# Kernel optimization log

Hardware: AMD Instinct MI355X
Metric: run time of the kernel (lower is better)

## Reference

```python
import jax, jax.numpy as jnp
import numpy as np

NUM_GRIDS = 8

def _rbf(x):
    # FastKAN-style radial basis over a fixed grid on [-2, 2]
    grid = jnp.linspace(-2.0, 2.0, NUM_GRIDS).astype(x.dtype)
    h = 4.0 / (NUM_GRIDS - 1)  # grid spacing used as RBF bandwidth
    z = (x[..., None] - grid) / h
    return jnp.exp(-z * z)  # (..., D, G)

def _spline_layer(x, base_w, base_b, spline_w, spline_b):
    # base path: Linear(silu(x)); spline path: Linear(rbf features)
    base = jax.nn.silu(x) @ base_w.T + base_b
    feats = _rbf(x).reshape(x.shape[:-1] + (x.shape[-1] * NUM_GRIDS,))
    return base + feats @ spline_w.T + spline_b


def setup_inputs() -> dict:
    key = jax.random.key(0)
    ks = jax.random.split(key, 12)
    B, Sx, Sy, D = 4, 1024, 1024, 256
    H1, H2 = 128, 64
    def lin(k, o, i):
        return (jax.random.normal(k, (o, i), jnp.float32) / np.sqrt(i)).astype(jnp.float32)
    return {
        "x": jax.random.normal(ks[0], (B, Sx, D), jnp.float32),
        "y": jax.random.normal(ks[1], (B, Sy, D), jnp.float32),
        "base_w1x": lin(ks[2], H1, D), "base_b1x": jnp.zeros((H1,), jnp.float32),
        "spline_w1x": lin(ks[3], H1, D * NUM_GRIDS), "spline_b1x": jnp.zeros((H1,), jnp.float32),
        "base_w2x": lin(ks[4], H2, H1), "base_b2x": jnp.zeros((H2,), jnp.float32),
        "spline_w2x": lin(ks[5], H2, H1 * NUM_GRIDS), "spline_b2x": jnp.zeros((H2,), jnp.float32),
        "base_w1y": lin(ks[6], H1, D), "base_b1y": jnp.zeros((H1,), jnp.float32),
        "spline_w1y": lin(ks[7], H1, D * NUM_GRIDS), "spline_b1y": jnp.zeros((H1,), jnp.float32),
        "base_w2y": lin(ks[8], H2, H1), "base_b2y": jnp.zeros((H2,), jnp.float32),
        "spline_w2y": lin(ks[9], H2, H1 * NUM_GRIDS), "spline_b2y": jnp.zeros((H2,), jnp.float32),
        "final_w": lin(ks[10], 1, 2 * H2), "final_b": jnp.zeros((1,), jnp.float32),
    }


def reference(x, y,
              base_w1x, base_b1x, spline_w1x, spline_b1x,
              base_w2x, base_b2x, spline_w2x, spline_b2x,
              base_w1y, base_b1y, spline_w1y, spline_b1y,
              base_w2y, base_b2y, spline_w2y, spline_b2y,
              final_w, final_b):
    # Per-branch spline stacks: (B, S, D) -> (B, S, H2)
    hx = _spline_layer(_spline_layer(x, base_w1x, base_b1x, spline_w1x, spline_b1x),
                       base_w2x, base_b2x, spline_w2x, spline_b2x)
    hy = _spline_layer(_spline_layer(y, base_w1y, base_b1y, spline_w1y, spline_b1y),
                       base_w2y, base_b2y, spline_w2y, spline_b2y)
    # The original expands to (B, Sx, Sy, 2*H2), applies the affine final
    # layer, then means over all Sx*Sy pairs. By linearity this equals two
    # independent seq-means projected by the split weight, avoiding the
    # quadratic intermediate while computing identical math.
    H2 = hx.shape[-1]
    wx, wy = final_w[:, :H2], final_w[:, H2:]
    out = hx.mean(axis=1) @ wx.T + hy.mean(axis=1) @ wy.T + final_b  # (B, 1)
    return out
```

## Files before the change

kernel.cpp:

```cpp
#include <hip/hip_runtime.h>

typedef __attribute__((ext_vector_type(8))) short short8;
typedef __attribute__((ext_vector_type(8))) float floatx8;
typedef __attribute__((ext_vector_type(8))) __bf16 bf16x8;
typedef __attribute__((ext_vector_type(16))) float floatx16;


__device__ __forceinline__ unsigned short f2bf(float f) {
  union { float f; unsigned u; } v; v.f = f;
  unsigned r = v.u + 0x7fffu + ((v.u >> 16) & 1u);
  return (unsigned short)(r >> 16);
}

#define STP 33

__global__ __launch_bounds__(256) void prep_frags(
    const float* __restrict__ bw1x, const float* __restrict__ sw1x,
    const float* __restrict__ bb1x, const float* __restrict__ sb1x,
    const float* __restrict__ bw2x, const float* __restrict__ sw2x,
    const float* __restrict__ bb2x, const float* __restrict__ sb2x,
    const float* __restrict__ bw1y, const float* __restrict__ sw1y,
    const float* __restrict__ bb1y, const float* __restrict__ sb1y,
    const float* __restrict__ bw2y, const float* __restrict__ sw2y,
    const float* __restrict__ bb2y, const float* __restrict__ sb2y,
    uint4* __restrict__ B1fx, uint4* __restrict__ B1fy,
    uint4* __restrict__ B2fx, uint4* __restrict__ B2fy,
    float* __restrict__ b1x, float* __restrict__ b1y,
    float* __restrict__ b2x, float* __restrict__ b2y,
    int* __restrict__ cnt)
{
  __shared__ unsigned short stage[9 * 16 * STP];

  const int cid = blockIdx.x;
  const int t   = threadIdx.x;

  if (cid < 160) {
    const bool isB1 = (cid < 128);
    int sid, ds, nc, ostr, sstr, ncs;
    const float *bw, *sw;
    uint4* dst;
    if (isB1) {
      sid = cid >> 6; int c = cid & 63; ds = c >> 2; nc = c & 3;
      bw = sid ? bw1y : bw1x; sw = sid ? sw1y : sw1x;
      dst = sid ? B1fy : B1fx;
      ostr = 256; sstr = 2048; ncs = 4;
    } else {
      int c2 = cid - 128; sid = c2 >> 4; int c = c2 & 15; ds = c >> 1; nc = c & 1;
      bw = sid ? bw2y : bw2x; sw = sid ? sw2y : sw2x;
      dst = sid ? B2fy : B2fx;
      ostr = 128; sstr = 1024; ncs = 2;
    }
    const int o_l = t >> 3;
    const int o   = nc * 32 + o_l;
    #pragma unroll
    for (int e = 0; e < 2; ++e) {
      int dd = (t & 7) * 2 + e;
      int d  = ds * 16 + dd;
      float bwv = bw[o * ostr + d];
      stage[(0 * 16 + dd) * STP + o_l] = f2bf(bwv);
      const float* sp = sw + (size_t)o * sstr + d * 8;
      float4 s0 = *(const float4*)sp;
      float4 s1 = *(const float4*)(sp + 4);
      stage[(1 * 16 + dd) * STP + o_l] = f2bf(s0.x);
      stage[(2 * 16 + dd) * STP + o_l] = f2bf(s0.y);
      stage[(3 * 16 + dd) * STP + o_l] = f2bf(s0.z);
      stage[(4 * 16 + dd) * STP + o_l] = f2bf(s0.w);
      stage[(5 * 16 + dd) * STP + o_l] = f2bf(s1.x);
      stage[(6 * 16 + dd) * STP + o_l] = f2bf(s1.y);
      stage[(7 * 16 + dd) * STP + o_l] = f2bf(s1.z);
      stage[(8 * 16 + dd) * STP + o_l] = f2bf(s1.w);
    }
    __syncthreads();
    for (int u = t; u < 9 * 64; u += 256) {
      int j = u >> 6, l = u & 63;
      int dd0 = (l >> 5) * 8;
      int oL  = l & 31;
      unsigned short e8[8];
      #pragma unroll
      for (int i = 0; i < 8; ++i)
        e8[i] = stage[(j * 16 + dd0 + i) * STP + oL];
      uint4 oh;
      oh.x = (unsigned)e8[0] | ((unsigned)e8[1] << 16);
      oh.y = (unsigned)e8[2] | ((unsigned)e8[3] << 16);
      oh.z = (unsigned)e8[4] | ((unsigned)e8[5] << 16);
      oh.w = (unsigned)e8[6] | ((unsigned)e8[7] << 16);
      int q = (ds * 9 + j) * ncs + nc;
      dst[q * 64 + l] = oh;
    }
  } else {
    for (int i2 = t; i2 < 388; i2 += 256) {
      if (i2 < 128)      b1x[i2]       = bb1x[i2]       + sb1x[i2];
      else if (i2 < 256) b1y[i2 - 128] = bb1y[i2 - 128] + sb1y[i2 - 128];
      else if (i2 < 320) b2x[i2 - 256] = bb2x[i2 - 256] + sb2x[i2 - 256];
      else if (i2 < 384) b2y[i2 - 320] = bb2y[i2 - 320] + sb2y[i2 - 320];
      else               cnt[i2 - 384] = 0;
    }
  }
}

__global__ __launch_bounds__(512, 2) void fused_kernel(
    const float* __restrict__ Xx, const float* __restrict__ Xy,
    const uint4* __restrict__ B1fx, const uint4* __restrict__ B1fy,
    const uint4* __restrict__ B2fx, const uint4* __restrict__ B2fy,
    const float* __restrict__ b1x_, const float* __restrict__ b1y_,
    const float* __restrict__ b2x_, const float* __restrict__ b2y_,
    const float* __restrict__ finw, const float* __restrict__ finb,
    float* __restrict__ partial, int* __restrict__ cnt,
    float* __restrict__ out)
{
  __shared__ __align__(16) char smem[51232];
  float* xsh  = (float*)smem;
  float* S0   = (float*)smem;
  float* S1   = (float*)(smem + 16384);
  float* h1s  = (float*)(smem + 33792);
  float* redw = (float*)(smem + 51200);

  const int t    = threadIdx.x;
  const int bid  = blockIdx.x;
  const int sid  = bid >> 7;
  const int m    = bid & 127;
  const int wave = t >> 6;
  const int l    = t & 63;
  const int lc   = l & 31;
  const int lk   = l >> 5;

  const float* X  = sid ? Xy : Xx;
  const uint4* B1 = sid ? B1fy : B1fx;
  const uint4* B2 = sid ? B2fy : B2fx;
  const float* b1 = sid ? b1y_ : b1x_;
  const float* b2 = sid ? b2y_ : b2x_;

  {
    int row = t >> 4, col = (t & 15) * 16;
    const float* src = X + (size_t)(m * 32 + row) * 256 + col;
    #pragma unroll
    for (int q = 0; q < 4; ++q)
      *(float4*)(xsh + row * 264 + col + q * 4) = *(const float4*)(src + q * 4);
  }
  __syncthreads();

  float xr0[8], xr1[8];
  {
    int cb = wave * 32 + lk * 8;
    float4 v0 = *(const float4*)(xsh + lc * 264 + cb);
    float4 v1 = *(const float4*)(xsh + lc * 264 + cb + 4);
    float4 u0 = *(const float4*)(xsh + lc * 264 + cb + 16);
    float4 u1 = *(const float4*)(xsh + lc * 264 + cb + 20);
    xr0[0]=v0.x; xr0[1]=v0.y; xr0[2]=v0.z; xr0[3]=v0.w;
    xr0[4]=v1.x; xr0[5]=v1.y; xr0[6]=v1.z; xr0[7]=v1.w;
    xr1[0]=u0.x; xr1[1]=u0.y; xr1[2]=u0.z; xr1[3]=u0.w;
    xr1[4]=u1.x; xr1[5]=u1.y; xr1[6]=u1.z; xr1[7]=u1.w;
  }
  __syncthreads();

  floatx16 acc[4] = {};

  auto loadB1 = [&](int s, uint4* bf) {
    int j = s >> 1, ds = wave * 2 + (s & 1);
    const uint4* bp = B1 + (size_t)((ds * 9 + j) * 4) * 64 + l;
    #pragma unroll
    for (int nc = 0; nc < 4; ++nc) bf[nc] = bp[nc * 64];
  };
  auto computeB1 = [&](int s, const uint4* bf) {
    int j = s >> 1;
    const float* xr = (s & 1) ? xr1 : xr0;
    floatx8 f;
    if (j == 0) {
      #pragma unroll
      for (int i = 0; i < 8; ++i)
        f[i] = __fdividef(xr[i], 1.f + __expf(-xr[i]));
    } else {
      float g = -2.f + (float)(j - 1) * (4.f / 7.f);
      #pragma unroll
      for (int i = 0; i < 8; ++i) {
        float z = (xr[i] - g) * 1.75f;
        f[i] = __expf(-z * z);
      }
    }
    short8 a = __builtin_bit_cast(short8, __builtin_convertvector(f, bf16x8));
    #pragma unroll
    for (int nc = 0; nc < 4; ++nc) {
      short8 bh = __builtin_bit_cast(short8, bf[nc]);
      acc[nc] = __builtin_amdgcn_mfma_f32_32x32x16_bf16(a, bh, acc[nc], 0, 0, 0);
    }
  };

  {
    uint4 bfE[4], bfO[4];
    loadB1(0, bfE);
    #pragma unroll 1
    for (int s = 0; s < 18; s += 2) {
      loadB1(s + 1, bfO);
      computeB1(s, bfE);
      if (s + 2 < 18) loadB1(s + 2, bfE);
      computeB1(s + 1, bfO);
    }
  }

  auto st = [&](float* Sb) {
    #pragma unroll
    for (int nc = 0; nc < 4; ++nc)
      #pragma unroll
      for (int r = 0; r < 16; ++r) {
        int row = (r & 3) + 8 * (r >> 2) + 4 * lk;
        Sb[row * 128 + nc * 32 + lc] = acc[nc][r];
      }
  };
  auto ad = [&](const float* Sb) {
    #pragma unroll
    for (int nc = 0; nc < 4; ++nc)
      #pragma unroll
      for (int r = 0; r < 16; ++r) {
        int row = (r & 3) + 8 * (r >> 2) + 4 * lk;
        acc[nc][r] += Sb[row * 128 + nc * 32 + lc];
      }
  };
  __syncthreads();
  if (wave == 1) st(S0);
  if (wave == 3) st(S1);
  __syncthreads();
  if (wave == 0) ad(S0);
  if (wave == 2) ad(S1);
  __syncthreads();
  if (wave == 5) st(S0);
  if (wave == 7) st(S1);
  __syncthreads();
  if (wave == 4) ad(S0);
  if (wave == 6) ad(S1);
  __syncthreads();
  if (wave == 2) st(S0);
  if (wave == 6) st(S1);
  __syncthreads();
  if (wave == 0) ad(S0);
  if (wave == 4) ad(S1);
  __syncthreads();
  if (wave == 4) st(S0);
  __syncthreads();
  if (wave == 0) {
    ad(S0);
    #pragma unroll
    for (int nc = 0; nc < 4; ++nc)
      #pragma unroll
      for (int r = 0; r < 16; ++r) {
        int row = (r & 3) + 8 * (r >> 2) + 4 * lk;
        int col = nc * 32 + lc;
        h1s[row * 136 + col] = acc[nc][r] + b1[col];
      }
  }
  __syncthreads();

  floatx16 acc2[2] = {};

  auto loadB2 = [&](int s, uint4* cf) {
    const uint4* bp = B2 + (size_t)((wave * 9 + s) * 2) * 64 + l;
    #pragma unroll
    for (int nc = 0; nc < 2; ++nc) cf[nc] = bp[nc * 64];
  };

  uint4 cfE[2], cfO[2];
  loadB2(0, cfE);

  float hr[8];
  {
    int cb = wave * 16 + lk * 8;
    float4 v0 = *(const float4*)(h1s + lc * 136 + cb);
    float4 v1 = *(const float4*)(h1s + lc * 136 + cb + 4);
    hr[0]=v0.x; hr[1]=v0.y; hr[2]=v0.z; hr[3]=v0.w;
    hr[4]=v1.x; hr[5]=v1.y; hr[6]=v1.z; hr[7]=v1.w;
  }

  auto computeB2 = [&](int s, const uint4* cf) {
    floatx8 f;
    if (s == 0) {
      #pragma unroll
      for (int i = 0; i < 8; ++i)
        f[i] = __fdividef(hr[i], 1.f + __expf(-hr[i]));
    } else {
      float g = -2.f + (float)(s - 1) * (4.f / 7.f);
      #pragma unroll
      for (int i = 0; i < 8; ++i) {
        float z = (hr[i] - g) * 1.75f;
        f[i] = __expf(-z * z);
      }
    }
    short8 a = __builtin_bit_cast(short8, __builtin_convertvector(f, bf16x8));
    #pragma unroll
    for (int nc = 0; nc < 2; ++nc) {
      short8 bh = __builtin_bit_cast(short8, cf[nc]);
      acc2[nc] = __builtin_amdgcn_mfma_f32_32x32x16_bf16(a, bh, acc2[nc], 0, 0, 0);
    }
  };

  #pragma unroll 1
  for (int s = 0; s < 8; s += 2) {
    loadB2(s + 1, cfO);
    computeB2(s, cfE);
    loadB2(s + 2, cfE);
    computeB2(s + 1, cfO);
  }
  computeB2(8, cfE);

  const float* wf = finw + sid * 64;
  {
    float w0 = wf[lc], w1v = wf[32 + lc];
    float pz = 0.f;
    #pragma unroll
    for (int r = 0; r < 16; ++r) pz += acc2[0][r] * w0 + acc2[1][r] * w1v;
    #pragma unroll
    for (int off = 32; off > 0; off >>= 1) pz += __shfl_down(pz, off, 64);
    if (l == 0) redw[wave] = pz;
  }
  __syncthreads();

  if (wave == 0) {
    const int b    = m >> 5;
    const int slot = sid * 32 + (m & 31);
    float v = (l < 8) ? redw[l] : 0.f;
    v += 32.f * b2[l] * wf[l];
    #pragma unroll
    for (int off = 32; off > 0; off >>= 1) v += __shfl_down(v, off, 64);
    int old = 0;
    if (l == 0) {
      partial[b * 64 + slot] = v;
      __threadfence();
      old = atomicAdd(&cnt[b], 1);
    }
    int bc = __shfl(old, 0, 64);
    if (bc == 63) {
      float pv = atomicAdd(&partial[b * 64 + l], 0.f);
      #pragma unroll
      for (int off = 32; off > 0; off >>= 1) pv += __shfl_down(pv, off, 64);
      if (l == 0) out[b] = finb[0] + pv * (1.0f / 1024.0f);
    }
  }
}

extern "C" void kernel_launch(void* const* d_in, const int* in_sizes, int n_in,
                              void* d_out, int out_size, void* d_ws, size_t ws_size,
                              hipStream_t stream)
{
  (void)in_sizes; (void)n_in; (void)out_size; (void)ws_size;
  const float* x    = (const float*)d_in[0];
  const float* y    = (const float*)d_in[1];
  const float* bw1x = (const float*)d_in[2];
  const float* bb1x = (const float*)d_in[3];
  const float* sw1x = (const float*)d_in[4];
  const float* sb1x = (const float*)d_in[5];
  const float* bw2x = (const float*)d_in[6];
  const float* bb2x = (const float*)d_in[7];
  const float* sw2x = (const float*)d_in[8];
  const float* sb2x = (const float*)d_in[9];
  const float* bw1y = (const float*)d_in[10];
  const float* bb1y = (const float*)d_in[11];
  const float* sw1y = (const float*)d_in[12];
  const float* sb1y = (const float*)d_in[13];
  const float* bw2y = (const float*)d_in[14];
  const float* bb2y = (const float*)d_in[15];
  const float* sw2y = (const float*)d_in[16];
  const float* sb2y = (const float*)d_in[17];
  const float* finw = (const float*)d_in[18];
  const float* finb = (const float*)d_in[19];

  char* ws = (char*)d_ws;
  uint4* B1fx = (uint4*)(ws);
  uint4* B1fy = (uint4*)(ws + 589824);
  uint4* B2fx = (uint4*)(ws + 1179648);
  uint4* B2fy = (uint4*)(ws + 1327104);
  float* b1x  = (float*)(ws + 1474560);
  float* b1y  = b1x + 128;
  float* b2x  = b1y + 128;
  float* b2y  = b2x + 64;
  float* partial = b2y + 64;
  int*   cnt  = (int*)(partial + 256);

  hipLaunchKernelGGL(prep_frags, dim3(161), dim3(256), 0, stream,
                     bw1x, sw1x, bb1x, sb1x, bw2x, sw2x, bb2x, sb2x,
                     bw1y, sw1y, bb1y, sb1y, bw2y, sw2y, bb2y, sb2y,
                     B1fx, B1fy, B2fx, B2fy, b1x, b1y, b2x, b2y, cnt);

  hipLaunchKernelGGL(fused_kernel, dim3(256), dim3(512), 0, stream,
                     x, y, B1fx, B1fy, B2fx, B2fy, b1x, b1y, b2x, b2y,
                     finw, finb, partial, cnt, (float*)d_out);
}
```

Before: 30.79 us.

## Drop B-fragment double-buffering and raise occupancy to three blocks per CU

Replaces the software-pipelined, double-buffered weight fragment loads in both MFMA loops with simple per-iteration load-then-compute loops. It also raises the launch-bounds minimum blocks per CU from 2 to 3. The aim is to cut register pressure so more waves are resident and can hide load latency through occupancy rather than manual prefetch. The risk is exposed global-load latency in each iteration if occupancy does not actually rise, or spills under the tighter register budget.

```diff
diff --git a/kernel.cpp b/kernel.cpp
--- a/kernel.cpp
+++ b/kernel.cpp
@@ -98,7 +98,7 @@
   }
 }
 
-__global__ __launch_bounds__(512, 2) void fused_kernel(
+__global__ __launch_bounds__(512, 3) void fused_kernel(
     const float* __restrict__ Xx, const float* __restrict__ Xy,
     const uint4* __restrict__ B1fx, const uint4* __restrict__ B1fy,
     const uint4* __restrict__ B2fx, const uint4* __restrict__ B2fy,
@@ -155,14 +155,14 @@
 
   floatx16 acc[4] = {};
 
-  auto loadB1 = [&](int s, uint4* bf) {
+  #pragma unroll 1
+  for (int s = 0; s < 18; ++s) {
     int j = s >> 1, ds = wave * 2 + (s & 1);
     const uint4* bp = B1 + (size_t)((ds * 9 + j) * 4) * 64 + l;
+    uint4 bf[4];
     #pragma unroll
     for (int nc = 0; nc < 4; ++nc) bf[nc] = bp[nc * 64];
-  };
-  auto computeB1 = [&](int s, const uint4* bf) {
-    int j = s >> 1;
+
     const float* xr = (s & 1) ? xr1 : xr0;
     floatx8 f;
     if (j == 0) {
@@ -183,18 +183,6 @@
       short8 bh = __builtin_bit_cast(short8, bf[nc]);
       acc[nc] = __builtin_amdgcn_mfma_f32_32x32x16_bf16(a, bh, acc[nc], 0, 0, 0);
     }
-  };
-
-  {
-    uint4 bfE[4], bfO[4];
-    loadB1(0, bfE);
-    #pragma unroll 1
-    for (int s = 0; s < 18; s += 2) {
-      loadB1(s + 1, bfO);
-      computeB1(s, bfE);
-      if (s + 2 < 18) loadB1(s + 2, bfE);
-      computeB1(s + 1, bfO);
-    }
   }
 
   auto st = [&](float* Sb) {
@@ -250,15 +238,6 @@
   __syncthreads();
 
   floatx16 acc2[2] = {};
-
-  auto loadB2 = [&](int s, uint4* cf) {
-    const uint4* bp = B2 + (size_t)((wave * 9 + s) * 2) * 64 + l;
-    #pragma unroll
-    for (int nc = 0; nc < 2; ++nc) cf[nc] = bp[nc * 64];
-  };
-
-  uint4 cfE[2], cfO[2];
-  loadB2(0, cfE);
 
   float hr[8];
   {
@@ -269,7 +248,13 @@
     hr[4]=v1.x; hr[5]=v1.y; hr[6]=v1.z; hr[7]=v1.w;
   }
 
-  auto computeB2 = [&](int s, const uint4* cf) {
+  #pragma unroll 1
+  for (int s = 0; s < 9; ++s) {
+    const uint4* bp = B2 + (size_t)((wave * 9 + s) * 2) * 64 + l;
+    uint4 cf[2];
+    #pragma unroll
+    for (int nc = 0; nc < 2; ++nc) cf[nc] = bp[nc * 64];
+
     floatx8 f;
     if (s == 0) {
       #pragma unroll
@@ -289,16 +274,7 @@
       short8 bh = __builtin_bit_cast(short8, cf[nc]);
       acc2[nc] = __builtin_amdgcn_mfma_f32_32x32x16_bf16(a, bh, acc2[nc], 0, 0, 0);
     }
-  };
-
-  #pragma unroll 1
-  for (int s = 0; s < 8; s += 2) {
-    loadB2(s + 1, cfO);
-    computeB2(s, cfE);
-    loadB2(s + 2, cfE);
-    computeB2(s + 1, cfO);
-  }
-  computeB2(8, cfE);
+  }
 
   const float* wf = finw + sid * 64;
   {
```

Result: slower. 32.26 us (+4.8%).
